# Kernel tuning notes

Measured on AMD Instinct MI355X. Metric: run time of the kernel, lower is better.

## Reference

```python
import jax, jax.numpy as jnp
import numpy as np

DIM_IN = 1024
DIM_K = 64
EPS = 1e-5

def setup_inputs() -> dict:
    key = jax.random.key(0)
    ks = jax.random.split(key, 9)
    s_in = 1.0 / np.sqrt(DIM_IN)
    s_k = 1.0 / np.sqrt(DIM_K)
    return {
        "X": jax.random.normal(ks[0], (8, 2048, DIM_IN), dtype=jnp.float32),
        "Wq": jax.random.uniform(ks[1], (DIM_IN, DIM_K), jnp.float32, -s_in, s_in),
        "bq": jax.random.uniform(ks[2], (DIM_K,), jnp.float32, -s_in, s_in),
        "Wk": jax.random.uniform(ks[3], (DIM_IN, DIM_K), jnp.float32, -s_in, s_in),
        "bk": jax.random.uniform(ks[4], (DIM_K,), jnp.float32, -s_in, s_in),
        "Wv": jax.random.uniform(ks[5], (DIM_IN, DIM_K), jnp.float32, -s_in, s_in),
        "bv": jax.random.uniform(ks[6], (DIM_K,), jnp.float32, -s_in, s_in),
        "Wo": jax.random.uniform(ks[7], (DIM_K, DIM_IN), jnp.float32, -s_k, s_k),
        "bo": jax.random.uniform(ks[8], (DIM_IN,), jnp.float32, -s_k, s_k),
        "gamma": jnp.ones((DIM_IN,), jnp.float32),
        "beta": jnp.zeros((DIM_IN,), jnp.float32),
    }

def reference(X, Wq, bq, Wk, bk, Wv, bv, Wo, bo, gamma, beta):
    q = X @ Wq + bq                       # [B,S,K]
    k = X @ Wk + bk
    v = X @ Wv + bv
    scores = jnp.einsum("bqk,bsk->bqs", q, k) / jnp.sqrt(jnp.float32(DIM_K))
    attn = jax.nn.softmax(scores, axis=2)  # [B,S,S]
    av = jnp.einsum("bqs,bsk->bqk", attn, v)
    y = X + av @ Wo + bo                  # residual, [B,S,D]
    mu = jnp.mean(y, axis=-1, keepdims=True)
    var = jnp.mean(jnp.square(y - mu), axis=-1, keepdims=True)
    return (y - mu) / jnp.sqrt(var + EPS) * gamma + beta
```

## Files before the change

kernel.cpp:

```cpp
#include <hip/hip_runtime.h>
#include <hip/hip_bf16.h>

#define DIM_D 1024
#define DIM_KH 64
#define SEQ   2048
#define BATCH 8
#define NROWS (BATCH*SEQ)
#define KVSPLIT 4
#define KEYS_PER_SPLIT (SEQ/KVSPLIT)

typedef __attribute__((ext_vector_type(8))) short short8;
typedef __attribute__((ext_vector_type(4))) short short4v;
typedef __attribute__((ext_vector_type(4))) float floatx4;

__device__ __forceinline__ ushort f2bf(float f) {
    union { __hip_bfloat16 h; ushort u; } cv;
    cv.h = __float2bfloat16(f);
    return cv.u;
}

__device__ __forceinline__ float bf2f(ushort u) {
    union { float f; uint u32; } c;
    c.u32 = (uint)u << 16;
    return c.f;
}

__device__ __forceinline__ uint4 pack8(float4 a, float4 b) {
    uint4 p;
    p.x = (uint)f2bf(a.x) | ((uint)f2bf(a.y) << 16);
    p.y = (uint)f2bf(a.z) | ((uint)f2bf(a.w) << 16);
    p.z = (uint)f2bf(b.x) | ((uint)f2bf(b.y) << 16);
    p.w = (uint)f2bf(b.z) | ((uint)f2bf(b.w) << 16);
    return p;
}

__global__ void wconv_all(const float* __restrict__ Wq,
                          const float* __restrict__ Wk,
                          const float* __restrict__ Wv,
                          const float* __restrict__ Wo,
                          ushort* __restrict__ WT,
                          ushort* __restrict__ WoT)
{
    const int tid = threadIdx.x;
    if (blockIdx.x < 192) {
        const int n  = blockIdx.x;
        const int o  = n >> 6;
        const int nn = n & 63;
        const float* W = (o == 0) ? Wq : (o == 1) ? Wk : Wv;
        #pragma unroll
        for (int i = 0; i < 4; i++) {
            int k = tid + i * 256;
            WT[(size_t)n * DIM_D + k] = f2bf(W[(size_t)k * DIM_KH + nn]);
        }
    } else {
        const int blk = blockIdx.x - 192;
        const int n = blk * 4 + (tid >> 6);
        const int k = tid & 63;
        WoT[(size_t)n * DIM_KH + k] = f2bf(Wo[(size_t)k * DIM_D + n]);
    }
}

__global__ __launch_bounds__(256, 1) void qkv_mfma(
    const float* __restrict__ X, const ushort* __restrict__ WT,
    const float* __restrict__ bq, const float* __restrict__ bk,
    const float* __restrict__ bv,
    ushort* __restrict__ Qb, ushort* __restrict__ Kb, ushort* __restrict__ Vb)
{
    const int tid = threadIdx.x;
    const int m0  = blockIdx.x * 64;
    const int o   = blockIdx.y;

    __shared__ ushort Xs[2][64 * 64];
    __shared__ ushort Wls[2][64 * 64];

    const int w  = tid >> 6;
    const int l  = tid & 63;
    const int ql = l & 15;
    const int g  = (l >> 4) & 3;
    const int swz = (ql & 7) << 3;

    const int sr  = tid >> 2;
    const int sc  = (tid & 3) << 4;
    const int ssw = (sr & 7) << 3;
    const float*  Xrow = X  + (size_t)(m0 + sr) * DIM_D + sc;
    const ushort* Wrow = WT + (size_t)(o * 64 + sr) * DIM_D + sc;

    float4 xr[4];
    uint4  wr[2];

    floatx4 acc[4];
    #pragma unroll
    for (int fn = 0; fn < 4; fn++) acc[fn] = (floatx4){0.f, 0.f, 0.f, 0.f};

    #pragma unroll
    for (int f = 0; f < 4; f++)
        xr[f] = *reinterpret_cast<const float4*>(Xrow + f * 4);
    #pragma unroll
    for (int h = 0; h < 2; h++)
        wr[h] = *reinterpret_cast<const uint4*>(Wrow + h * 8);
    #pragma unroll
    for (int h = 0; h < 2; h++) {
        *reinterpret_cast<uint4*>(&Xs[0][sr * 64 + ((sc + h * 8) ^ ssw)]) =
            pack8(xr[2 * h], xr[2 * h + 1]);
        *reinterpret_cast<uint4*>(&Wls[0][sr * 64 + ((sc + h * 8) ^ ssw)]) = wr[h];
    }
    __syncthreads();

    #pragma unroll
    for (int t = 0; t < 16; t++) {
        const int cur = t & 1;
        const int nxt = cur ^ 1;
        if (t < 15) {
            const int k1 = (t + 1) * 64;
            #pragma unroll
            for (int f = 0; f < 4; f++)
                xr[f] = *reinterpret_cast<const float4*>(Xrow + k1 + f * 4);
            #pragma unroll
            for (int h = 0; h < 2; h++)
                wr[h] = *reinterpret_cast<const uint4*>(Wrow + k1 + h * 8);
        }

        #pragma unroll
        for (int kk = 0; kk < 2; kk++) {
            short8 a = *reinterpret_cast<const short8*>(
                &Xs[cur][(16 * w + ql) * 64 + ((kk * 32 + g * 8) ^ swz)]);
            #pragma unroll
            for (int fn = 0; fn < 4; fn++) {
                short8 b = *reinterpret_cast<const short8*>(
                    &Wls[cur][(16 * fn + ql) * 64 + ((kk * 32 + g * 8) ^ swz)]);
                acc[fn] = __builtin_amdgcn_mfma_f32_16x16x32_bf16(a, b, acc[fn], 0, 0, 0);
            }
        }

        if (t < 15) {
            #pragma unroll
            for (int h = 0; h < 2; h++) {
                *reinterpret_cast<uint4*>(&Xs[nxt][sr * 64 + ((sc + h * 8) ^ ssw)]) =
                    pack8(xr[2 * h], xr[2 * h + 1]);
                *reinterpret_cast<uint4*>(&Wls[nxt][sr * 64 + ((sc + h * 8) ^ ssw)]) = wr[h];
            }
        }
        __syncthreads();
    }

    const float* bias = (o == 0) ? bq : (o == 1) ? bk : bv;
    ushort* O = (o == 0) ? Qb : (o == 1) ? Kb : Vb;
    float bvreg[4];
    #pragma unroll
    for (int fn = 0; fn < 4; fn++) bvreg[fn] = bias[16 * fn + ql];

    #pragma unroll
    for (int fn = 0; fn < 4; fn++) {
        #pragma unroll
        for (int r = 0; r < 4; r++) {
            int row = m0 + 16 * w + 4 * g + r;
            O[(size_t)row * DIM_KH + 16 * fn + ql] = f2bf(acc[fn][r] + bvreg[fn]);
        }
    }
}

__global__ __launch_bounds__(256) void attn_mfma(
    const ushort* __restrict__ Qb, const ushort* __restrict__ Kb,
    const ushort* __restrict__ Vb,
    ushort* __restrict__ OpartB, float* __restrict__ Ml)
{
    const int tid = threadIdx.x;
    const int w   = tid >> 6;
    const int l   = tid & 63;
    const int ql  = l & 15;
    const int g   = (l >> 4) & 3;
    const int q0  = blockIdx.x * 64;
    const int s   = blockIdx.y;
    const int b   = blockIdx.z;
    const int swzq = (ql & 7) << 3;

    __shared__ ushort Ks[64 * 64];
    __shared__ ushort VTs[64 * 64];

    short8 qf[2];
    #pragma unroll
    for (int kk = 0; kk < 2; kk++) {
        qf[kk] = *reinterpret_cast<const short8*>(
            Qb + ((size_t)(b * SEQ + q0 + 16 * w + ql)) * DIM_KH + kk * 32 + g * 8);
    }

    floatx4 accv[4];
    #pragma unroll
    for (int fd = 0; fd < 4; fd++) accv[fd] = (floatx4){0.f, 0.f, 0.f, 0.f};
    float m_run = -3.0e38f, l_run = 0.f;

    const ushort* Kbb = Kb + (size_t)b * SEQ * DIM_KH;
    const ushort* Vbb = Vb + (size_t)b * SEQ * DIM_KH;
    const int t_begin = s * KEYS_PER_SPLIT;
    const int t_end   = t_begin + KEYS_PER_SPLIT;

    for (int t0 = t_begin; t0 < t_end; t0 += 64) {
        __syncthreads();
        #pragma unroll
        for (int i = 0; i < 2; i++) {
            int idx = tid + i * 256;
            int row = idx >> 3;
            int ch  = idx & 7;
            uint4 v = *reinterpret_cast<const uint4*>(
                Kbb + (size_t)(t0 + row) * DIM_KH + ch * 8);
            *reinterpret_cast<uint4*>(&Ks[row * 64 + ((ch * 8) ^ ((row & 7) << 3))]) = v;
        }
        {
            int kg = tid >> 4, dg = tid & 15;
            int key0 = kg * 4, dim0 = dg * 4;
            uint2 vr[4];
            #pragma unroll
            for (int i = 0; i < 4; i++)
                vr[i] = *reinterpret_cast<const uint2*>(
                    Vbb + (size_t)(t0 + key0 + i) * DIM_KH + dim0);
            #pragma unroll
            for (int j = 0; j < 4; j++) {
                uint e0 = (j == 0) ? (vr[0].x & 0xffffu) : (j == 1) ? (vr[0].x >> 16)
                        : (j == 2) ? (vr[0].y & 0xffffu) : (vr[0].y >> 16);
                uint e1 = (j == 0) ? (vr[1].x & 0xffffu) : (j == 1) ? (vr[1].x >> 16)
                        : (j == 2) ? (vr[1].y & 0xffffu) : (vr[1].y >> 16);
                uint e2 = (j == 0) ? (vr[2].x & 0xffffu) : (j == 1) ? (vr[2].x >> 16)
                        : (j == 2) ? (vr[2].y & 0xffffu) : (vr[2].y >> 16);
                uint e3 = (j == 0) ? (vr[3].x & 0xffffu) : (j == 1) ? (vr[3].x >> 16)
                        : (j == 2) ? (vr[3].y & 0xffffu) : (vr[3].y >> 16);
                uint2 p; p.x = e0 | (e1 << 16); p.y = e2 | (e3 << 16);
                int dim = dim0 + j;
                int addr = dim * 64 + (key0 ^ ((dim & 15) << 2));
                *reinterpret_cast<uint2*>(&VTs[addr]) = p;
            }
        }
        __syncthreads();

        floatx4 sfrag[4];
        #pragma unroll
        for (int f = 0; f < 4; f++) {
            sfrag[f] = (floatx4){0.f, 0.f, 0.f, 0.f};
            #pragma unroll
            for (int kk = 0; kk < 2; kk++) {
                short8 a = *reinterpret_cast<const short8*>(
                    &Ks[(16 * f + ql) * 64 + ((kk * 32 + g * 8) ^ swzq)]);
                sfrag[f] = __builtin_amdgcn_mfma_f32_16x16x32_bf16(a, qf[kk], sfrag[f], 0, 0, 0);
            }
        }

        float mt = -3.0e38f;
        #pragma unroll
        for (int f = 0; f < 4; f++)
            #pragma unroll
            for (int r = 0; r < 4; r++) mt = fmaxf(mt, sfrag[f][r]);
        mt = fmaxf(mt, __shfl_xor(mt, 16));
        mt = fmaxf(mt, __shfl_xor(mt, 32));
        float m_new = fmaxf(m_run, mt);
        float sc = __expf((m_run - m_new) * 0.125f);
        float psum = 0.f;
        ushort pb[4][4];
        #pragma unroll
        for (int f = 0; f < 4; f++)
            #pragma unroll
            for (int r = 0; r < 4; r++) {
                float p = __expf((sfrag[f][r] - m_new) * 0.125f);
                pb[f][r] = f2bf(p);
                psum += p;
            }
        psum += __shfl_xor(psum, 16);
        psum += __shfl_xor(psum, 32);
        l_run = l_run * sc + psum;
        m_run = m_new;

        float s0 = __shfl(sc, 4 * g + 0);
        float s1 = __shfl(sc, 4 * g + 1);
        float s2 = __shfl(sc, 4 * g + 2);
        float s3 = __shfl(sc, 4 * g + 3);
        #pragma unroll
        for (int fd = 0; fd < 4; fd++) {
            accv[fd][0] *= s0; accv[fd][1] *= s1;
            accv[fd][2] *= s2; accv[fd][3] *= s3;
        }

        short8 pa_lo, pa_hi;
        pa_lo[0] = (short)pb[0][0]; pa_lo[1] = (short)pb[0][1];
        pa_lo[2] = (short)pb[0][2]; pa_lo[3] = (short)pb[0][3];
        pa_lo[4] = (short)pb[1][0]; pa_lo[5] = (short)pb[1][1];
        pa_lo[6] = (short)pb[1][2]; pa_lo[7] = (short)pb[1][3];
        pa_hi[0] = (short)pb[2][0]; pa_hi[1] = (short)pb[2][1];
        pa_hi[2] = (short)pb[2][2]; pa_hi[3] = (short)pb[2][3];
        pa_hi[4] = (short)pb[3][0]; pa_hi[5] = (short)pb[3][1];
        pa_hi[6] = (short)pb[3][2]; pa_hi[7] = (short)pb[3][3];

        #pragma unroll
        for (int fd = 0; fd < 4; fd++) {
            int dim = 16 * fd + ql;
            int base = dim * 64;
            int sw = (dim & 15) << 2;
            short4v v0 = *reinterpret_cast<const short4v*>(&VTs[base + ((4 * g) ^ sw)]);
            short4v v1 = *reinterpret_cast<const short4v*>(&VTs[base + ((16 + 4 * g) ^ sw)]);
            short8 bb;
            bb[0] = v0[0]; bb[1] = v0[1]; bb[2] = v0[2]; bb[3] = v0[3];
            bb[4] = v1[0]; bb[5] = v1[1]; bb[6] = v1[2]; bb[7] = v1[3];
            accv[fd] = __builtin_amdgcn_mfma_f32_16x16x32_bf16(pa_lo, bb, accv[fd], 0, 0, 0);
            short4v v2 = *reinterpret_cast<const short4v*>(&VTs[base + ((32 + 4 * g) ^ sw)]);
            short4v v3 = *reinterpret_cast<const short4v*>(&VTs[base + ((48 + 4 * g) ^ sw)]);
            short8 bb2;
            bb2[0] = v2[0]; bb2[1] = v2[1]; bb2[2] = v2[2]; bb2[3] = v2[3];
            bb2[4] = v3[0]; bb2[5] = v3[1]; bb2[6] = v3[2]; bb2[7] = v3[3];
            accv[fd] = __builtin_amdgcn_mfma_f32_16x16x32_bf16(pa_hi, bb2, accv[fd], 0, 0, 0);
        }
    }

    const size_t rid0 = (size_t)b * SEQ + q0;
    if (g == 0) {
        size_t rid = rid0 + 16 * w + ql;
        Ml[((size_t)s * NROWS + rid) * 2 + 0] = m_run;
        Ml[((size_t)s * NROWS + rid) * 2 + 1] = l_run;
    }
    #pragma unroll
    for (int fd = 0; fd < 4; fd++) {
        int col = 16 * fd + ql;
        size_t rbase = (size_t)s * NROWS + rid0 + 16 * w + 4 * g;
        OpartB[(rbase + 0) * DIM_KH + col] = f2bf(accv[fd][0]);
        OpartB[(rbase + 1) * DIM_KH + col] = f2bf(accv[fd][1]);
        OpartB[(rbase + 2) * DIM_KH + col] = f2bf(accv[fd][2]);
        OpartB[(rbase + 3) * DIM_KH + col] = f2bf(accv[fd][3]);
    }
}

__global__ __launch_bounds__(256, 1) void out_mfma(
    const float* __restrict__ X, const ushort* __restrict__ OpartB,
    const float* __restrict__ Ml,
    const ushort* __restrict__ WoT, const float* __restrict__ bo,
    const float* __restrict__ gamma, const float* __restrict__ beta,
    float* __restrict__ Out)
{
    const int tid = threadIdx.x;
    const int w   = tid >> 6;
    const int l   = tid & 63;
    const int ql  = l & 15;
    const int g   = (l >> 4) & 3;
    const int row0 = blockIdx.x * 16;
    const int c0  = w * 256;

    __shared__ ushort Ls[16 * 1024];

    const int r  = tid >> 4;
    const int cb = (tid & 15) * 4;
    const float* Xrow = X + (size_t)(row0 + r) * DIM_D;
    float4 xv[16];
    #pragma unroll
    for (int j = 0; j < 16; j++)
        xv[j] = *reinterpret_cast<const float4*>(Xrow + cb + 64 * j);

    const size_t rid = (size_t)row0 + ql;
    float m[KVSPLIT], lv[KVSPLIT];
    float M = -3.0e38f;
    #pragma unroll
    for (int s = 0; s < KVSPLIT; s++) {
        float2 t = *reinterpret_cast<const float2*>(Ml + ((size_t)s * NROWS + rid) * 2);
        m[s] = t.x; lv[s] = t.y;
        M = fmaxf(M, m[s]);
    }
    float wsum = 0.f;
    float o[16];
    #pragma unroll
    for (int d = 0; d < 16; d++) o[d] = 0.f;
    #pragma unroll
    for (int s = 0; s < KVSPLIT; s++) {
        float wgt = __expf((m[s] - M) * 0.125f);
        wsum = fmaf(wgt, lv[s], wsum);
        const ushort* op = OpartB + ((size_t)s * NROWS + rid) * DIM_KH;
        union { uint4 u; ushort us[8]; } a, b;
        a.u = *reinterpret_cast<const uint4*>(op + g * 8);
        b.u = *reinterpret_cast<const uint4*>(op + 32 + g * 8);
        #pragma unroll
        for (int j = 0; j < 8; j++) {
            o[j]     = fmaf(wgt, bf2f(a.us[j]), o[j]);
            o[8 + j] = fmaf(wgt, bf2f(b.us[j]), o[8 + j]);
        }
    }
    float avinv = 1.0f / wsum;
    short8 bf0, bf1;
    #pragma unroll
    for (int j = 0; j < 8; j++) {
        bf0[j] = (short)f2bf(o[j] * avinv);
        bf1[j] = (short)f2bf(o[8 + j] * avinv);
    }

    const ushort* apb = WoT + (size_t)(c0 + ql) * DIM_KH + g * 8;
    short8 a0c = *reinterpret_cast<const short8*>(apb);
    short8 a1c = *reinterpret_cast<const short8*>(apb + 32);
    #pragma unroll
    for (int ft = 0; ft < 16; ft++) {
        short8 a0n, a1n;
        if (ft < 15) {
            const ushort* apn = apb + (size_t)(ft + 1) * 16 * DIM_KH;
            a0n = *reinterpret_cast<const short8*>(apn);
            a1n = *reinterpret_cast<const short8*>(apn + 32);
        }
        floatx4 z = (floatx4){0.f, 0.f, 0.f, 0.f};
        z = __builtin_amdgcn_mfma_f32_16x16x32_bf16(a0c, bf0, z, 0, 0, 0);
        z = __builtin_amdgcn_mfma_f32_16x16x32_bf16(a1c, bf1, z, 0, 0, 0);
        int col = (c0 + 16 * ft + 4 * g) ^ ((ql & 7) << 2);
        uint2 p;
        p.x = (uint)f2bf(z[0]) | ((uint)f2bf(z[1]) << 16);
        p.y = (uint)f2bf(z[2]) | ((uint)f2bf(z[3]) << 16);
        *reinterpret_cast<uint2*>(&Ls[ql * 1024 + col]) = p;
        if (ft < 15) { a0c = a0n; a1c = a1n; }
    }
    __syncthreads();

    const int rsw = (r & 7) << 2;

    float4 yv[16];
    float s = 0.f, sq = 0.f;
    #pragma unroll
    for (int j = 0; j < 16; j++) {
        int col = cb + 64 * j;
        union { uint2 u; ushort us[4]; } a;
        a.u = *reinterpret_cast<const uint2*>(&Ls[r * 1024 + (col ^ rsw)]);
        float4 b4 = *reinterpret_cast<const float4*>(bo + col);
        float y0 = bf2f(a.us[0]) + xv[j].x + b4.x;
        float y1 = bf2f(a.us[1]) + xv[j].y + b4.y;
        float y2 = bf2f(a.us[2]) + xv[j].z + b4.z;
        float y3 = bf2f(a.us[3]) + xv[j].w + b4.w;
        yv[j] = (float4){y0, y1, y2, y3};
        s  += (y0 + y1) + (y2 + y3);
        sq += fmaf(y0, y0, fmaf(y1, y1, fmaf(y2, y2, y3 * y3)));
    }
    s  += __shfl_xor(s, 1);  s  += __shfl_xor(s, 2);
    s  += __shfl_xor(s, 4);  s  += __shfl_xor(s, 8);
    sq += __shfl_xor(sq, 1); sq += __shfl_xor(sq, 2);
    sq += __shfl_xor(sq, 4); sq += __shfl_xor(sq, 8);

    float mu  = s * (1.0f / 1024.0f);
    float var = fmaf(sq, (1.0f / 1024.0f), -mu * mu);
    float inv = rsqrtf(var + 1e-5f);

    float* Orow = Out + (size_t)(row0 + r) * DIM_D;
    #pragma unroll
    for (int j = 0; j < 16; j++) {
        int col = cb + 64 * j;
        float4 g4  = *reinterpret_cast<const float4*>(gamma + col);
        float4 be4 = *reinterpret_cast<const float4*>(beta + col);
        float4 ov;
        ov.x = fmaf((yv[j].x - mu) * inv, g4.x, be4.x);
        ov.y = fmaf((yv[j].y - mu) * inv, g4.y, be4.y);
        ov.z = fmaf((yv[j].z - mu) * inv, g4.z, be4.z);
        ov.w = fmaf((yv[j].w - mu) * inv, g4.w, be4.w);
        *reinterpret_cast<float4*>(Orow + col) = ov;
    }
}

extern "C" void kernel_launch(void* const* d_in, const int* in_sizes, int n_in,
                              void* d_out, int out_size, void* d_ws, size_t ws_size,
                              hipStream_t stream)
{
    (void)in_sizes; (void)n_in; (void)out_size; (void)ws_size;
    const float* X     = (const float*)d_in[0];
    const float* Wq    = (const float*)d_in[1];
    const float* bq    = (const float*)d_in[2];
    const float* Wk    = (const float*)d_in[3];
    const float* bk    = (const float*)d_in[4];
    const float* Wv    = (const float*)d_in[5];
    const float* bv    = (const float*)d_in[6];
    const float* Wo    = (const float*)d_in[7];
    const float* bo    = (const float*)d_in[8];
    const float* gamma = (const float*)d_in[9];
    const float* beta  = (const float*)d_in[10];
    float* Out = (float*)d_out;

    ushort* Qb  = (ushort*)d_ws;
    ushort* Kb  = Qb + (size_t)NROWS * DIM_KH;
    ushort* Vb  = Kb + (size_t)NROWS * DIM_KH;
    ushort* WT  = Vb + (size_t)NROWS * DIM_KH;
    ushort* WoT = WT + (size_t)192 * DIM_D;
    ushort* OpartB = WoT + (size_t)DIM_D * DIM_KH;
    float*  Ml  = (float*)(OpartB + (size_t)KVSPLIT * NROWS * DIM_KH);

    wconv_all<<<448, 256, 0, stream>>>(Wq, Wk, Wv, Wo, WT, WoT);
    qkv_mfma<<<dim3(256, 3), 256, 0, stream>>>(X, WT, bq, bk, bv, Qb, Kb, Vb);
    attn_mfma<<<dim3(SEQ/64, KVSPLIT, BATCH), 256, 0, stream>>>(Qb, Kb, Vb, OpartB, Ml);
    out_mfma<<<NROWS/16, 256, 0, stream>>>(X, OpartB, Ml, WoT, bo, gamma, beta, Out);
}
```

Baseline: 94.31 us.

## Double-buffer K/V tiles in attention kernel with register prefetch

The attention kernel now keeps two LDS buffers for K and transposed V. The next tile is loaded into registers before computing on the current tile and written to the alternate buffer afterwards, which removes one barrier per iteration. The aim is to hide global load latency behind the MFMA and softmax work. In exchange it doubles LDS use to 32KB per block and raises register pressure, which may lower occupancy.

```diff
diff --git a/kernel.cpp b/kernel.cpp
--- a/kernel.cpp
+++ b/kernel.cpp
@@ -174,8 +174,13 @@
     const int b   = blockIdx.z;
     const int swzq = (ql & 7) << 3;
 
-    __shared__ ushort Ks[64 * 64];
-    __shared__ ushort VTs[64 * 64];
+    __shared__ ushort Ks[2][64 * 64];
+    __shared__ ushort VTs[2][64 * 64];
+
+    const int krow0 = tid >> 3;
+    const int kch   = tid & 7;
+    const int kg    = tid >> 4, dg = tid & 15;
+    const int key0  = kg * 4, dim0 = dg * 4;
 
     short8 qf[2];
     #pragma unroll
@@ -192,27 +197,144 @@
     const ushort* Kbb = Kb + (size_t)b * SEQ * DIM_KH;
     const ushort* Vbb = Vb + (size_t)b * SEQ * DIM_KH;
     const int t_begin = s * KEYS_PER_SPLIT;
-    const int t_end   = t_begin + KEYS_PER_SPLIT;
-
-    for (int t0 = t_begin; t0 < t_end; t0 += 64) {
-        __syncthreads();
-        #pragma unroll
-        for (int i = 0; i < 2; i++) {
-            int idx = tid + i * 256;
-            int row = idx >> 3;
-            int ch  = idx & 7;
-            uint4 v = *reinterpret_cast<const uint4*>(
-                Kbb + (size_t)(t0 + row) * DIM_KH + ch * 8);
-            *reinterpret_cast<uint4*>(&Ks[row * 64 + ((ch * 8) ^ ((row & 7) << 3))]) = v;
-        }
-        {
-            int kg = tid >> 4, dg = tid & 15;
-            int key0 = kg * 4, dim0 = dg * 4;
-            uint2 vr[4];
+    const int NT = KEYS_PER_SPLIT / 64;
+
+    uint4 kr[2];
+    uint2 vr[4];
+
+    #pragma unroll
+    for (int i = 0; i < 2; i++) {
+        int row = (tid + i * 256) >> 3;
+        kr[i] = *reinterpret_cast<const uint4*>(
+            Kbb + (size_t)(t_begin + row) * DIM_KH + kch * 8);
+    }
+    #pragma unroll
+    for (int i = 0; i < 4; i++)
+        vr[i] = *reinterpret_cast<const uint2*>(
+            Vbb + (size_t)(t_begin + key0 + i) * DIM_KH + dim0);
+    #pragma unroll
+    for (int i = 0; i < 2; i++) {
+        int row = (tid + i * 256) >> 3;
+        *reinterpret_cast<uint4*>(
+            &Ks[0][row * 64 + ((kch * 8) ^ ((row & 7) << 3))]) = kr[i];
+    }
+    #pragma unroll
+    for (int j = 0; j < 4; j++) {
+        uint e0 = (j == 0) ? (vr[0].x & 0xffffu) : (j == 1) ? (vr[0].x >> 16)
+                : (j == 2) ? (vr[0].y & 0xffffu) : (vr[0].y >> 16);
+        uint e1 = (j == 0) ? (vr[1].x & 0xffffu) : (j == 1) ? (vr[1].x >> 16)
+                : (j == 2) ? (vr[1].y & 0xffffu) : (vr[1].y >> 16);
+        uint e2 = (j == 0) ? (vr[2].x & 0xffffu) : (j == 1) ? (vr[2].x >> 16)
+                : (j == 2) ? (vr[2].y & 0xffffu) : (vr[2].y >> 16);
+        uint e3 = (j == 0) ? (vr[3].x & 0xffffu) : (j == 1) ? (vr[3].x >> 16)
+                : (j == 2) ? (vr[3].y & 0xffffu) : (vr[3].y >> 16);
+        uint2 p; p.x = e0 | (e1 << 16); p.y = e2 | (e3 << 16);
+        int dim = dim0 + j;
+        *reinterpret_cast<uint2*>(
+            &VTs[0][dim * 64 + (key0 ^ ((dim & 15) << 2))]) = p;
+    }
+    __syncthreads();
+
+    for (int ti = 0; ti < NT; ti++) {
+        const int cur = ti & 1;
+        const int nxt = cur ^ 1;
+
+        if (ti < NT - 1) {
+            const int t1 = t_begin + (ti + 1) * 64;
+            #pragma unroll
+            for (int i = 0; i < 2; i++) {
+                int row = (tid + i * 256) >> 3;
+                kr[i] = *reinterpret_cast<const uint4*>(
+                    Kbb + (size_t)(t1 + row) * DIM_KH + kch * 8);
+            }
             #pragma unroll
             for (int i = 0; i < 4; i++)
                 vr[i] = *reinterpret_cast<const uint2*>(
-                    Vbb + (size_t)(t0 + key0 + i) * DIM_KH + dim0);
+                    Vbb + (size_t)(t1 + key0 + i) * DIM_KH + dim0);
+        }
+
+        floatx4 sfrag[4];
+        #pragma unroll
+        for (int f = 0; f < 4; f++) {
+            sfrag[f] = (floatx4){0.f, 0.f, 0.f, 0.f};
+            #pragma unroll
+            for (int kk = 0; kk < 2; kk++) {
+                short8 a = *reinterpret_cast<const short8*>(
+                    &Ks[cur][(16 * f + ql) * 64 + ((kk * 32 + g * 8) ^ swzq)]);
+                sfrag[f] = __builtin_amdgcn_mfma_f32_16x16x32_bf16(a, qf[kk], sfrag[f], 0, 0, 0);
+            }
+        }
+
+        float mt = -3.0e38f;
+        #pragma unroll
+        for (int f = 0; f < 4; f++)
+            #pragma unroll
+            for (int r = 0; r < 4; r++) mt = fmaxf(mt, sfrag[f][r]);
+        mt = fmaxf(mt, __shfl_xor(mt, 16));
+        mt = fmaxf(mt, __shfl_xor(mt, 32));
+        float m_new = fmaxf(m_run, mt);
+        float sc = __expf((m_run - m_new) * 0.125f);
+        float psum = 0.f;
+        ushort pb[4][4];
+        #pragma unroll
+        for (int f = 0; f < 4; f++)
+            #pragma unroll
+            for (int r = 0; r < 4; r++) {
+                float p = __expf((sfrag[f][r] - m_new) * 0.125f);
+                pb[f][r] = f2bf(p);
+                psum += p;
+            }
+        psum += __shfl_xor(psum, 16);
+        psum += __shfl_xor(psum, 32);
+        l_run = l_run * sc + psum;
+        m_run = m_new;
+
+        float s0 = __shfl(sc, 4 * g + 0);
+        float s1 = __shfl(sc, 4 * g + 1);
+        float s2 = __shfl(sc, 4 * g + 2);
+        float s3 = __shfl(sc, 4 * g + 3);
+        #pragma unroll
+        for (int fd = 0; fd < 4; fd++) {
+            accv[fd][0] *= s0; accv[fd][1] *= s1;
+            accv[fd][2] *= s2; accv[fd][3] *= s3;
+        }
+
+        short8 pa_lo, pa_hi;
+        pa_lo[0] = (short)pb[0][0]; pa_lo[1] = (short)pb[0][1];
+        pa_lo[2] = (short)pb[0][2]; pa_lo[3] = (short)pb[0][3];
+        pa_lo[4] = (short)pb[1][0]; pa_lo[5] = (short)pb[1][1];
+        pa_lo[6] = (short)pb[1][2]; pa_lo[7] = (short)pb[1][3];
+        pa_hi[0] = (short)pb[2][0]; pa_hi[1] = (short)pb[2][1];
+        pa_hi[2] = (short)pb[2][2]; pa_hi[3] = (short)pb[2][3];
+        pa_hi[4] = (short)pb[3][0]; pa_hi[5] = (short)pb[3][1];
+        pa_hi[6] = (short)pb[3][2]; pa_hi[7] = (short)pb[3][3];
+
+        #pragma unroll
+        for (int fd = 0; fd < 4; fd++) {
+            int dim = 16 * fd + ql;
+            int base = dim * 64;
+            int sw = (dim & 15) << 2;
+            short4v v0 = *reinterpret_cast<const short4v*>(&VTs[cur][base + ((4 * g) ^ sw)]);
+            short4v v1 = *reinterpret_cast<const short4v*>(&VTs[cur][base + ((16 + 4 * g) ^ sw)]);
+            short8 bb;
+            bb[0] = v0[0]; bb[1] = v0[1]; bb[2] = v0[2]; bb[3] = v0[3];
+            bb[4] = v1[0]; bb[5] = v1[1]; bb[6] = v1[2]; bb[7] = v1[3];
+            accv[fd] = __builtin_amdgcn_mfma_f32_16x16x32_bf16(pa_lo, bb, accv[fd], 0, 0, 0);
+            short4v v2 = *reinterpret_cast<const short4v*>(&VTs[cur][base + ((32 + 4 * g) ^ sw)]);
+            short4v v3 = *reinterpret_cast<const short4v*>(&VTs[cur][base + ((48 + 4 * g) ^ sw)]);
+            short8 bb2;
+            bb2[0] = v2[0]; bb2[1] = v2[1]; bb2[2] = v2[2]; bb2[3] = v2[3];
+            bb2[4] = v3[0]; bb2[5] = v3[1]; bb2[6] = v3[2]; bb2[7] = v3[3];
+            accv[fd] = __builtin_amdgcn_mfma_f32_16x16x32_bf16(pa_hi, bb2, accv[fd], 0, 0, 0);
+        }
+
+        if (ti < NT - 1) {
+            #pragma unroll
+            for (int i = 0; i < 2; i++) {
+                int row = (tid + i * 256) >> 3;
+                *reinterpret_cast<uint4*>(
+                    &Ks[nxt][row * 64 + ((kch * 8) ^ ((row & 7) << 3))]) = kr[i];
+            }
             #pragma unroll
             for (int j = 0; j < 4; j++) {
                 uint e0 = (j == 0) ? (vr[0].x & 0xffffu) : (j == 1) ? (vr[0].x >> 16)
@@ -225,86 +347,11 @@
                         : (j == 2) ? (vr[3].y & 0xffffu) : (vr[3].y >> 16);
                 uint2 p; p.x = e0 | (e1 << 16); p.y = e2 | (e3 << 16);
                 int dim = dim0 + j;
-                int addr = dim * 64 + (key0 ^ ((dim & 15) << 2));
-                *reinterpret_cast<uint2*>(&VTs[addr]) = p;
+                *reinterpret_cast<uint2*>(
+                    &VTs[nxt][dim * 64 + (key0 ^ ((dim & 15) << 2))]) = p;
             }
         }
         __syncthreads();
-
-        floatx4 sfrag[4];
-        #pragma unroll
-        for (int f = 0; f < 4; f++) {
-            sfrag[f] = (floatx4){0.f, 0.f, 0.f, 0.f};
-            #pragma unroll
-            for (int kk = 0; kk < 2; kk++) {
-                short8 a = *reinterpret_cast<const short8*>(
-                    &Ks[(16 * f + ql) * 64 + ((kk * 32 + g * 8) ^ swzq)]);
-                sfrag[f] = __builtin_amdgcn_mfma_f32_16x16x32_bf16(a, qf[kk], sfrag[f], 0, 0, 0);
-            }
-        }
-
-        float mt = -3.0e38f;
-        #pragma unroll
-        for (int f = 0; f < 4; f++)
-            #pragma unroll
-            for (int r = 0; r < 4; r++) mt = fmaxf(mt, sfrag[f][r]);
-        mt = fmaxf(mt, __shfl_xor(mt, 16));
-        mt = fmaxf(mt, __shfl_xor(mt, 32));
-        float m_new = fmaxf(m_run, mt);
-        float sc = __expf((m_run - m_new) * 0.125f);
-        float psum = 0.f;
-        ushort pb[4][4];
-        #pragma unroll
-        for (int f = 0; f < 4; f++)
-            #pragma unroll
-            for (int r = 0; r < 4; r++) {
-                float p = __expf((sfrag[f][r] - m_new) * 0.125f);
-                pb[f][r] = f2bf(p);
-                psum += p;
-            }
-        psum += __shfl_xor(psum, 16);
-        psum += __shfl_xor(psum, 32);
-        l_run = l_run * sc + psum;
-        m_run = m_new;
-
-        float s0 = __shfl(sc, 4 * g + 0);
-        float s1 = __shfl(sc, 4 * g + 1);
-        float s2 = __shfl(sc, 4 * g + 2);
-        float s3 = __shfl(sc, 4 * g + 3);
-        #pragma unroll
-        for (int fd = 0; fd < 4; fd++) {
-            accv[fd][0] *= s0; accv[fd][1] *= s1;
-            accv[fd][2] *= s2; accv[fd][3] *= s3;
-        }
-
-        short8 pa_lo, pa_hi;
-        pa_lo[0] = (short)pb[0][0]; pa_lo[1] = (short)pb[0][1];
-        pa_lo[2] = (short)pb[0][2]; pa_lo[3] = (short)pb[0][3];
-        pa_lo[4] = (short)pb[1][0]; pa_lo[5] = (short)pb[1][1];
-        pa_lo[6] = (short)pb[1][2]; pa_lo[7] = (short)pb[1][3];
-        pa_hi[0] = (short)pb[2][0]; pa_hi[1] = (short)pb[2][1];
-        pa_hi[2] = (short)pb[2][2]; pa_hi[3] = (short)pb[2][3];
-        pa_hi[4] = (short)pb[3][0]; pa_hi[5] = (short)pb[3][1];
-        pa_hi[6] = (short)pb[3][2]; pa_hi[7] = (short)pb[3][3];
-
-        #pragma unroll
-        for (int fd = 0; fd < 4; fd++) {
-            int dim = 16 * fd + ql;
-            int base = dim * 64;
-            int sw = (dim & 15) << 2;
-            short4v v0 = *reinterpret_cast<const short4v*>(&VTs[base + ((4 * g) ^ sw)]);
-            short4v v1 = *reinterpret_cast<const short4v*>(&VTs[base + ((16 + 4 * g) ^ sw)]);
-            short8 bb;
-            bb[0] = v0[0]; bb[1] = v0[1]; bb[2] = v0[2]; bb[3] = v0[3];
-            bb[4] = v1[0]; bb[5] = v1[1]; bb[6] = v1[2]; bb[7] = v1[3];
-            accv[fd] = __builtin_amdgcn_mfma_f32_16x16x32_bf16(pa_lo, bb, accv[fd], 0, 0, 0);
-            short4v v2 = *reinterpret_cast<const short4v*>(&VTs[base + ((32 + 4 * g) ^ sw)]);
-            short4v v3 = *reinterpret_cast<const short4v*>(&VTs[base + ((48 + 4 * g) ^ sw)]);
-            short8 bb2;
-            bb2[0] = v2[0]; bb2[1] = v2[1]; bb2[2] = v2[2]; bb2[3] = v2[3];
-            bb2[4] = v3[0]; bb2[5] = v3[1]; bb2[6] = v3[2]; bb2[7] = v3[3];
-            accv[fd] = __builtin_amdgcn_mfma_f32_16x16x32_bf16(pa_hi, bb2, accv[fd], 0, 0, 0);
-        }
     }
 
     const size_t rid0 = (size_t)b * SEQ + q0;
```

Measured after the change: 93.84 us. Within noise of the previous version (-0.5%).
